# Kernel optimization log

Measured on AMD Instinct MI355X. Metric: run time of the kernel, lower is better.

The kernel has to match this reference:

```python
import jax, jax.numpy as jnp
import numpy as np
import math

INPUT_DIM = 256
HIDDEN_DIM = 128  # per-head dim
NUM_HEAD = 8
N = 1024          # seq len == variables
BATCH = 8
C = HIDDEN_DIM * NUM_HEAD  # 1024


def setup_inputs() -> dict:
    key = jax.random.key(0)
    ks = jax.random.split(key, 11)
    s = 0.02
    return {
        "x": jax.random.normal(ks[0], (BATCH, N, INPUT_DIM), dtype=jnp.float32),
        "B_bias": jax.random.normal(ks[1], (N, N), dtype=jnp.float32),
        "wq_w": jax.random.normal(ks[2], (INPUT_DIM, C), dtype=jnp.float32) * s,
        "wq_b": jax.random.normal(ks[3], (C,), dtype=jnp.float32) * s,
        "wk_w": jax.random.normal(ks[4], (INPUT_DIM, C), dtype=jnp.float32) * s,
        "wk_b": jax.random.normal(ks[5], (C,), dtype=jnp.float32) * s,
        "wv_w": jax.random.normal(ks[6], (INPUT_DIM, C), dtype=jnp.float32) * s,
        "wv_b": jax.random.normal(ks[7], (C,), dtype=jnp.float32) * s,
        "proj_w": jax.random.normal(ks[8], (C, HIDDEN_DIM), dtype=jnp.float32) * s,
        "proj_b": jax.random.normal(ks[9], (HIDDEN_DIM,), dtype=jnp.float32) * s,
    }


def reference(x, B_bias, wq_w, wq_b, wk_w, wk_b, wv_w, wv_b, proj_w, proj_b):
    B, n, _ = x.shape
    sdk = jnp.float32(math.sqrt(HIDDEN_DIM))
    # projections -> [B, N, C], split heads -> [B, H, N, h]
    def heads(y):
        return y.reshape(B, n, NUM_HEAD, HIDDEN_DIM).transpose(0, 2, 1, 3)
    q = heads(x @ wq_w + wq_b)
    k = heads(x @ wk_w + wk_b)
    v = heads(x @ wv_w + wv_b)
    # scores [B, H, N, N] with learned additive bias (broadcast over B, H)
    scores = jnp.einsum("bhnd,bhmd->bhnm", q, k) / sdk + B_bias
    attn = jax.nn.softmax(scores, axis=-1)
    out = jnp.einsum("bhnm,bhmd->bhnd", attn, v)  # [B, H, N, h]
    out = out.transpose(0, 2, 1, 3).reshape(B, n, C)
    return out @ proj_w + proj_b
```

## Files before the change

### kernel.cpp

```cpp
#include <hip/hip_runtime.h>
#include <math.h>

#define SEQ  1024
#define IND  256
#define CC   1024
#define NH   8
#define HD   128
#define BH   64

typedef __bf16 bf16x8 __attribute__((ext_vector_type(8)));
typedef __bf16 bf16x4 __attribute__((ext_vector_type(4)));
typedef float  f32x4  __attribute__((ext_vector_type(4)));
typedef unsigned short u16;

static constexpr float RSDK = 0.08838834764831845f;

__device__ __forceinline__ u16 f2bf(float f) {
    unsigned int u = __float_as_uint(f);
    u += 0x7fffu + ((u >> 16) & 1u);
    return (u16)(u >> 16);
}

__device__ __forceinline__ unsigned cvt_pk_bf16(float lo, float hi) {
    unsigned r;
    asm("v_cvt_pk_bf16_f32 %0, %1, %2" : "=v"(r) : "v"(lo), "v"(hi));
    return r;
}

__global__ __launch_bounds__(256) void prep_kernel(
    const float* __restrict__ x, u16* __restrict__ xb,
    const float* __restrict__ w0, const float* __restrict__ w1, const float* __restrict__ w2,
    u16* __restrict__ o0, u16* __restrict__ o1, u16* __restrict__ o2,
    const float* __restrict__ pw, u16* __restrict__ pT)
{
    __shared__ float tile[32][33];
    const int id = blockIdx.x;

    if (id < 2048) {
        const int i = id * 256 + threadIdx.x;
        float4 v = ((const float4*)x)[i];
        ushort4 o;
        o.x = f2bf(v.x); o.y = f2bf(v.y); o.z = f2bf(v.z); o.w = f2bf(v.w);
        ((ushort4*)xb)[i] = o;
        return;
    }

    const float* in; u16* out; int R, C, c0, r0;
    if (id < 2816) {
        const int rem = id - 2048;
        const int z = rem >> 8;
        const int rem2 = rem & 255;
        in  = (z == 0) ? w0 : (z == 1) ? w1 : w2;
        out = (z == 0) ? o0 : (z == 1) ? o1 : o2;
        R = IND; C = CC;
        c0 = (rem2 & 31) * 32;
        r0 = (rem2 >> 5) * 32;
    } else {
        const int rem = id - 2816;
        in = pw; out = pT;
        R = CC; C = HD;
        c0 = (rem & 3) * 32;
        r0 = (rem >> 2) * 32;
    }

    const int row = threadIdx.x >> 3, col4 = (threadIdx.x & 7) * 4;
    float4 v = *(const float4*)&in[(size_t)(r0 + row) * C + c0 + col4];
    tile[row][col4 + 0] = v.x; tile[row][col4 + 1] = v.y;
    tile[row][col4 + 2] = v.z; tile[row][col4 + 3] = v.w;
    __syncthreads();
    ushort4 o;
    o.x = f2bf(tile[col4 + 0][row]);
    o.y = f2bf(tile[col4 + 1][row]);
    o.z = f2bf(tile[col4 + 2][row]);
    o.w = f2bf(tile[col4 + 3][row]);
    *(ushort4*)&out[(size_t)(c0 + row) * R + r0 + col4] = o;
}

#define QKV_LDW 72
__global__ __launch_bounds__(256) void qkv_kernel(
    const u16* __restrict__ xb,
    const u16* __restrict__ wT0, const u16* __restrict__ wT1, const u16* __restrict__ wT2,
    const float* __restrict__ b0, const float* __restrict__ b1, const float* __restrict__ b2,
    u16* __restrict__ q_out, u16* __restrict__ k_out, u16* __restrict__ vt_out)
{
    const int mat = blockIdx.z;
    const u16* wT  = (mat == 0) ? wT0 : (mat == 1) ? wT1 : wT2;
    const float* wb = (mat == 0) ? b0 : (mat == 1) ? b1 : b2;
    const float scale = (mat == 0) ? RSDK : 1.0f;

    __shared__ __align__(16) u16 As[128 * QKV_LDW];
    __shared__ __align__(16) u16 Bs[128 * QKV_LDW];

    const int tid = threadIdx.x;
    const int lane = tid & 63, wave = tid >> 6;
    const int ln = lane & 15, quad = lane >> 4;
    const int m0 = blockIdx.x * 128;
    const int n0 = blockIdx.y * 128;
    const int wm = (wave & 1) * 64;
    const int wn = (wave >> 1) * 64;

    f32x4 acc[4][4];
    #pragma unroll
    for (int mb = 0; mb < 4; ++mb)
        #pragma unroll
        for (int nb = 0; nb < 4; ++nb)
            #pragma unroll
            for (int r = 0; r < 4; ++r) acc[mb][nb][r] = 0.0f;

    const int r8 = tid >> 3, pb8 = tid & 7;

    const u16* ag = xb + (size_t)(m0 + r8) * IND + pb8 * 8;
    const u16* bg = wT + (size_t)(n0 + r8) * IND + pb8 * 8;

    bf16x8 pa[4], pbv[4];
    #pragma unroll
    for (int c = 0; c < 4; ++c) {
        pa[c]  = *(const bf16x8*)(ag + (size_t)c * 32 * IND);
        pbv[c] = *(const bf16x8*)(bg + (size_t)c * 32 * IND);
    }

    for (int kt = 0; kt < 4; ++kt) {
        __syncthreads();
        #pragma unroll
        for (int c = 0; c < 4; ++c) {
            *(bf16x8*)(As + (size_t)(c * 32 + r8) * QKV_LDW + pb8 * 8) = pa[c];
            *(bf16x8*)(Bs + (size_t)(c * 32 + r8) * QKV_LDW + pb8 * 8) = pbv[c];
        }
        __syncthreads();
        if (kt < 3) {
            #pragma unroll
            for (int c = 0; c < 4; ++c) {
                pa[c]  = *(const bf16x8*)(ag + (size_t)c * 32 * IND + (kt + 1) * 64);
                pbv[c] = *(const bf16x8*)(bg + (size_t)c * 32 * IND + (kt + 1) * 64);
            }
        }
        #pragma unroll
        for (int ks = 0; ks < 2; ++ks) {
            bf16x8 af[4], bf[4];
            #pragma unroll
            for (int mb = 0; mb < 4; ++mb)
                af[mb] = *(const bf16x8*)(As + (size_t)(wm + mb * 16 + ln) * QKV_LDW
                                             + (ks * 4 + quad) * 8);
            #pragma unroll
            for (int nb = 0; nb < 4; ++nb)
                bf[nb] = *(const bf16x8*)(Bs + (size_t)(wn + nb * 16 + ln) * QKV_LDW
                                             + (ks * 4 + quad) * 8);
            #pragma unroll
            for (int mb = 0; mb < 4; ++mb)
                #pragma unroll
                for (int nb = 0; nb < 4; ++nb)
                    acc[mb][nb] = __builtin_amdgcn_mfma_f32_16x16x32_bf16(
                        af[mb], bf[nb], acc[mb][nb], 0, 0, 0);
        }
    }

    if (mat != 2) {
        u16* outp = (mat == 0) ? q_out : k_out;
        #pragma unroll
        for (int nb = 0; nb < 4; ++nb) {
            const int c = n0 + wn + nb * 16 + ln;
            const float bv = wb[c];
            const int h = c >> 7, d = c & 127;
            #pragma unroll
            for (int mb = 0; mb < 4; ++mb) {
                #pragma unroll
                for (int r = 0; r < 4; ++r) {
                    const int m = m0 + wm + mb * 16 + quad * 4 + r;
                    const int b = m >> 10, tok = m & 1023;
                    outp[((size_t)(b * NH + h) * SEQ + tok) * HD + d] =
                        f2bf((acc[mb][nb][r] + bv) * scale);
                }
            }
        }
    } else {
        #pragma unroll
        for (int nb = 0; nb < 4; ++nb) {
            const int c = n0 + wn + nb * 16 + ln;
            const float bv = wb[c];
            const int h = c >> 7, d = c & 127;
            #pragma unroll
            for (int mb = 0; mb < 4; ++mb) {
                const int m = m0 + wm + mb * 16 + quad * 4;
                const int b = m >> 10, tok0 = m & 1023;
                ushort4 o;
                o.x = f2bf(acc[mb][nb][0] + bv);
                o.y = f2bf(acc[mb][nb][1] + bv);
                o.z = f2bf(acc[mb][nb][2] + bv);
                o.w = f2bf(acc[mb][nb][3] + bv);
                *(ushort4*)&vt_out[((size_t)(b * NH + h) * HD + d) * SEQ + tok0] = o;
            }
        }
    }
}

#define KVB    32
#define KS_LDW 136
#define VS_LDW 40
__global__ __launch_bounds__(256, 2) void attn_kernel(
    const u16* __restrict__ Q, const u16* __restrict__ K,
    const u16* __restrict__ Vt, const float* __restrict__ bias,
    u16* __restrict__ aout)
{
    __shared__ __align__(16) u16 Ks[KVB * KS_LDW];
    __shared__ __align__(16) u16 Vs[128 * VS_LDW];

    const int tid = threadIdx.x;
    const int lane = tid & 63, wave = tid >> 6;
    const int ln = lane & 15, quad = lane >> 4;
    const int bh = blockIdx.x;
    const int q0 = blockIdx.y * 128 + wave * 32;

    bf16x8 qf[2][4];
    #pragma unroll
    for (int mb = 0; mb < 2; ++mb) {
        const u16* qp = Q + ((size_t)bh * SEQ + q0 + mb * 16 + ln) * HD + quad * 8;
        #pragma unroll
        for (int ks = 0; ks < 4; ++ks) qf[mb][ks] = *(const bf16x8*)(qp + ks * 32);
    }

    f32x4 Oa[2][8];
    #pragma unroll
    for (int mb = 0; mb < 2; ++mb)
        #pragma unroll
        for (int db = 0; db < 8; ++db)
            #pragma unroll
            for (int r = 0; r < 4; ++r) Oa[mb][db][r] = 0.0f;
    float l_loc[2] = {0.0f, 0.0f};

    const u16* Kg0 = K  + (size_t)bh * SEQ * HD;
    const u16* Vg0 = Vt + (size_t)bh * HD * SEQ;
    const float* brow0 = bias + (size_t)(q0 + ln) * SEQ + quad * 4;
    const float* brow1 = brow0 + (size_t)16 * SEQ;

    const int r16 = tid >> 4, pb16 = tid & 15;
    const int r4  = tid >> 2, pb4  = tid & 3;

    const u16* kg = Kg0 + (size_t)r16 * HD + pb16 * 8;
    const u16* vg = Vg0 + (size_t)r4 * SEQ + pb4 * 8;

    bf16x8 kp[2], vp[2];
    #pragma unroll
    for (int c = 0; c < 2; ++c) {
        kp[c] = *(const bf16x8*)(kg + (size_t)c * 16 * HD);
        vp[c] = *(const bf16x8*)(vg + (size_t)c * 64 * SEQ);
    }

    float4 bpre[2][2];
    #pragma unroll
    for (int mb = 0; mb < 2; ++mb)
        #pragma unroll
        for (int nb = 0; nb < 2; ++nb)
            bpre[mb][nb] = *(const float4*)((mb ? brow1 : brow0) + nb * 16);

    for (int kt = 0; kt < 32; ++kt) {
        __syncthreads();
        #pragma unroll
        for (int c = 0; c < 2; ++c) {
            *(bf16x8*)(Ks + (size_t)(c * 16 + r16) * KS_LDW + pb16 * 8) = kp[c];
            *(bf16x8*)(Vs + (size_t)(c * 64 + r4) * VS_LDW + pb4 * 8)   = vp[c];
        }
        __syncthreads();

        if (kt < 31) {
            #pragma unroll
            for (int c = 0; c < 2; ++c) {
                kp[c] = *(const bf16x8*)(kg + (size_t)(kt + 1) * KVB * HD + (size_t)c * 16 * HD);
                vp[c] = *(const bf16x8*)(vg + (size_t)c * 64 * SEQ + (kt + 1) * KVB);
            }
        }

        float p8[2][2][4];
        #pragma unroll
        for (int nb = 0; nb < 2; ++nb) {
            const u16* kr = Ks + (size_t)(nb * 16 + ln) * KS_LDW;
            bf16x8 kf[4];
            #pragma unroll
            for (int ks = 0; ks < 4; ++ks)
                kf[ks] = *(const bf16x8*)(kr + (ks * 4 + quad) * 8);
            #pragma unroll
            for (int mb = 0; mb < 2; ++mb) {
                f32x4 s;
                #pragma unroll
                for (int r = 0; r < 4; ++r) s[r] = 0.0f;
                #pragma unroll
                for (int ks = 0; ks < 4; ++ks)
                    s = __builtin_amdgcn_mfma_f32_16x16x32_bf16(kf[ks], qf[mb][ks], s, 0, 0, 0);
                #pragma unroll
                for (int r = 0; r < 4; ++r) {
                    const float p = __expf(s[r] + bpre[mb][nb][r]);
                    l_loc[mb] += p;
                    p8[mb][nb][r] = p;
                }
            }
        }

        if (kt < 31) {
            #pragma unroll
            for (int mb = 0; mb < 2; ++mb)
                #pragma unroll
                for (int nb = 0; nb < 2; ++nb)
                    bpre[mb][nb] = *(const float4*)((mb ? brow1 : brow0)
                                                    + (kt + 1) * KVB + nb * 16);
        }

        bf16x8 af[2];
        #pragma unroll
        for (int mb = 0; mb < 2; ++mb) {
            unsigned x0 = cvt_pk_bf16(p8[mb][0][0], p8[mb][0][1]);
            unsigned x1 = cvt_pk_bf16(p8[mb][0][2], p8[mb][0][3]);
            unsigned y0 = cvt_pk_bf16(p8[mb][1][0], p8[mb][1][1]);
            unsigned y1 = cvt_pk_bf16(p8[mb][1][2], p8[mb][1][3]);
            asm("v_permlane32_swap_b32 %0, %1" : "+v"(x0), "+v"(y0));
            asm("v_permlane32_swap_b32 %0, %1" : "+v"(x1), "+v"(y1));
            asm("v_permlane16_swap_b32 %0, %1" : "+v"(x0), "+v"(y0));
            asm("v_permlane16_swap_b32 %0, %1" : "+v"(x1), "+v"(y1));
            union { unsigned u[4]; bf16x8 v; } afu;
            afu.u[0] = x0; afu.u[1] = x1; afu.u[2] = y0; afu.u[3] = y1;
            af[mb] = afu.v;
        }

        #pragma unroll
        for (int db = 0; db < 8; ++db) {
            bf16x8 vf = *(const bf16x8*)(Vs + (size_t)(db * 16 + ln) * VS_LDW + quad * 8);
            #pragma unroll
            for (int mb = 0; mb < 2; ++mb)
                Oa[mb][db] = __builtin_amdgcn_mfma_f32_16x16x32_bf16(
                    af[mb], vf, Oa[mb][db], 0, 0, 0);
        }
    }

    const int b = bh >> 3, h = bh & 7;
    #pragma unroll
    for (int mb = 0; mb < 2; ++mb) {
        float ltot = l_loc[mb];
        ltot += __shfl_xor(ltot, 16);
        ltot += __shfl_xor(ltot, 32);
        #pragma unroll
        for (int r = 0; r < 4; ++r) {
            const float inv = 1.0f / __shfl(ltot, quad * 4 + r);
            const int tok = q0 + mb * 16 + quad * 4 + r;
            u16* op = aout + ((size_t)(b * SEQ + tok)) * CC + h * HD + ln;
            #pragma unroll
            for (int db = 0; db < 8; ++db) op[db * 16] = f2bf(Oa[mb][db][r] * inv);
        }
    }
}

__global__ __launch_bounds__(256) void proj_kernel(
    const u16* __restrict__ A, const u16* __restrict__ pT,
    const float* __restrict__ pb, float* __restrict__ out)
{
    __shared__ float Rs[3][16 * 132];
    const int tid = threadIdx.x;
    const int lane = tid & 63, kh = tid >> 6;
    const int ln = lane & 15, quad = lane >> 4;
    const int m0 = blockIdx.x * 16;

    f32x4 acc[8];
    #pragma unroll
    for (int nb = 0; nb < 8; ++nb)
        #pragma unroll
        for (int r = 0; r < 4; ++r) acc[nb][r] = 0.0f;

    const u16* ap = A  + (size_t)(m0 + ln) * CC + kh * 256 + quad * 8;
    const u16* bp = pT + (size_t)ln * CC + kh * 256 + quad * 8;

    #pragma unroll
    for (int kt = 0; kt < 8; ++kt) {
        bf16x8 af = *(const bf16x8*)(ap + kt * 32);
        #pragma unroll
        for (int nb = 0; nb < 8; ++nb) {
            bf16x8 bf = *(const bf16x8*)(bp + (size_t)nb * 16 * CC + kt * 32);
            acc[nb] = __builtin_amdgcn_mfma_f32_16x16x32_bf16(af, bf, acc[nb], 0, 0, 0);
        }
    }

    if (kh > 0) {
        #pragma unroll
        for (int nb = 0; nb < 8; ++nb)
            #pragma unroll
            for (int r = 0; r < 4; ++r)
                Rs[kh - 1][(quad * 4 + r) * 132 + nb * 16 + ln] = acc[nb][r];
    }
    __syncthreads();
    if (kh == 0) {
        #pragma unroll
        for (int nb = 0; nb < 8; ++nb) {
            const int c = nb * 16 + ln;
            const float bv = pb[c];
            #pragma unroll
            for (int r = 0; r < 4; ++r) {
                const int ri = (quad * 4 + r) * 132 + c;
                out[(size_t)(m0 + quad * 4 + r) * HD + c] =
                    acc[nb][r] + Rs[0][ri] + Rs[1][ri] + Rs[2][ri] + bv;
            }
        }
    }
}

extern "C" void kernel_launch(void* const* d_in, const int* in_sizes, int n_in,
                              void* d_out, int out_size, void* d_ws, size_t ws_size,
                              hipStream_t stream)
{
    const float* x    = (const float*)d_in[0];
    const float* bias = (const float*)d_in[1];
    const float* wq   = (const float*)d_in[2];
    const float* wqb  = (const float*)d_in[3];
    const float* wk   = (const float*)d_in[4];
    const float* wkb  = (const float*)d_in[5];
    const float* wv   = (const float*)d_in[6];
    const float* wvb  = (const float*)d_in[7];
    const float* pw   = (const float*)d_in[8];
    const float* pb   = (const float*)d_in[9];
    float* out = (float*)d_out;

    u16* ws = (u16*)d_ws;
    size_t off = 0;
    u16* xb  = ws + off; off += (size_t)8192 * IND;
    u16* wqT = ws + off; off += (size_t)CC * IND;
    u16* wkT = ws + off; off += (size_t)CC * IND;
    u16* wvT = ws + off; off += (size_t)CC * IND;
    u16* pT  = ws + off; off += (size_t)HD * CC;
    u16* Qw  = ws + off; off += (size_t)BH * SEQ * HD;
    u16* Kw  = ws + off; off += (size_t)BH * SEQ * HD;
    u16* Vtw = ws + off; off += (size_t)BH * HD * SEQ;
    u16* Aw  = ws + off; off += (size_t)8192 * CC;

    prep_kernel<<<2944, 256, 0, stream>>>(x, xb, wq, wk, wv, wqT, wkT, wvT, pw, pT);
    qkv_kernel<<<dim3(64, 8, 3), 256, 0, stream>>>(
        xb, wqT, wkT, wvT, wqb, wkb, wvb, Qw, Kw, Vtw);
    attn_kernel<<<dim3(64, 8), 256, 0, stream>>>(Qw, Kw, Vtw, bias, Aw);
    proj_kernel<<<512, 256, 0, stream>>>(Aw, pT, pb, out);
}
```

Baseline: 172.1 us.

## Split attention KV loop across two wave groups and merge partial outputs in LDS

The attention block doubles to 512 threads, with two groups of four waves each handling alternating KV tiles over the same query rows. This halves the serial KV loop per wave and adds more waves for latency hiding. At the end, group 1 writes its partial O and row sums to shared memory and group 0 adds them before the store. The change relies on the softmax having no max subtraction, so partials add directly. It costs a reduction through LDS and tighter register limits under launch_bounds(512,4).

```diff
diff --git a/kernel.cpp b/kernel.cpp
--- a/kernel.cpp
+++ b/kernel.cpp
@@ -196,19 +196,25 @@
 #define KVB    32
 #define KS_LDW 136
 #define VS_LDW 40
-__global__ __launch_bounds__(256, 2) void attn_kernel(
+#define KS_SZ  (KVB * KS_LDW)
+#define VS_SZ  (128 * VS_LDW)
+__global__ __launch_bounds__(512, 4) void attn_kernel(
     const u16* __restrict__ Q, const u16* __restrict__ K,
     const u16* __restrict__ Vt, const float* __restrict__ bias,
     u16* __restrict__ aout)
 {
-    __shared__ __align__(16) u16 Ks[KVB * KS_LDW];
-    __shared__ __align__(16) u16 Vs[128 * VS_LDW];
+    __shared__ __align__(16) u16 SM[2 * KS_SZ + 2 * VS_SZ];
 
     const int tid = threadIdx.x;
     const int lane = tid & 63, wave = tid >> 6;
     const int ln = lane & 15, quad = lane >> 4;
+    const int g  = wave >> 2;
+    const int wq = wave & 3;
     const int bh = blockIdx.x;
-    const int q0 = blockIdx.y * 128 + wave * 32;
+    const int q0 = blockIdx.y * 128 + wq * 32;
+
+    u16* Ksg = SM + g * KS_SZ;
+    u16* Vsg = SM + 2 * KS_SZ + g * VS_SZ;
 
     bf16x8 qf[2][4];
     #pragma unroll
@@ -232,47 +238,46 @@
     const float* brow0 = bias + (size_t)(q0 + ln) * SEQ + quad * 4;
     const float* brow1 = brow0 + (size_t)16 * SEQ;
 
-    const int r16 = tid >> 4, pb16 = tid & 15;
-    const int r4  = tid >> 2, pb4  = tid & 3;
+    const int st = tid & 255;
+    const int r16 = st >> 4, pb16 = st & 15;
+    const int r4  = st >> 2, pb4  = st & 3;
 
     const u16* kg = Kg0 + (size_t)r16 * HD + pb16 * 8;
     const u16* vg = Vg0 + (size_t)r4 * SEQ + pb4 * 8;
 
     bf16x8 kp[2], vp[2];
-    #pragma unroll
-    for (int c = 0; c < 2; ++c) {
-        kp[c] = *(const bf16x8*)(kg + (size_t)c * 16 * HD);
-        vp[c] = *(const bf16x8*)(vg + (size_t)c * 64 * SEQ);
-    }
+    kp[0] = *(const bf16x8*)(kg + (size_t)g * KVB * HD);
+    kp[1] = *(const bf16x8*)(kg + (size_t)g * KVB * HD + (size_t)16 * HD);
+    vp[0] = *(const bf16x8*)(vg + g * KVB);
+    vp[1] = *(const bf16x8*)(vg + (size_t)64 * SEQ + g * KVB);
 
     float4 bpre[2][2];
     #pragma unroll
     for (int mb = 0; mb < 2; ++mb)
         #pragma unroll
         for (int nb = 0; nb < 2; ++nb)
-            bpre[mb][nb] = *(const float4*)((mb ? brow1 : brow0) + nb * 16);
-
-    for (int kt = 0; kt < 32; ++kt) {
-        __syncthreads();
-        #pragma unroll
-        for (int c = 0; c < 2; ++c) {
-            *(bf16x8*)(Ks + (size_t)(c * 16 + r16) * KS_LDW + pb16 * 8) = kp[c];
-            *(bf16x8*)(Vs + (size_t)(c * 64 + r4) * VS_LDW + pb4 * 8)   = vp[c];
-        }
-        __syncthreads();
-
-        if (kt < 31) {
-            #pragma unroll
-            for (int c = 0; c < 2; ++c) {
-                kp[c] = *(const bf16x8*)(kg + (size_t)(kt + 1) * KVB * HD + (size_t)c * 16 * HD);
-                vp[c] = *(const bf16x8*)(vg + (size_t)c * 64 * SEQ + (kt + 1) * KVB);
-            }
+            bpre[mb][nb] = *(const float4*)((mb ? brow1 : brow0) + g * KVB + nb * 16);
+
+    for (int i = 0; i < 16; ++i) {
+        __syncthreads();
+        *(bf16x8*)(Ksg + (size_t)r16 * KS_LDW + pb16 * 8)        = kp[0];
+        *(bf16x8*)(Ksg + (size_t)(16 + r16) * KS_LDW + pb16 * 8) = kp[1];
+        *(bf16x8*)(Vsg + (size_t)r4 * VS_LDW + pb4 * 8)          = vp[0];
+        *(bf16x8*)(Vsg + (size_t)(64 + r4) * VS_LDW + pb4 * 8)   = vp[1];
+        __syncthreads();
+
+        if (i < 15) {
+            const size_t t = (size_t)(2 * (i + 1) + g);
+            kp[0] = *(const bf16x8*)(kg + t * KVB * HD);
+            kp[1] = *(const bf16x8*)(kg + t * KVB * HD + (size_t)16 * HD);
+            vp[0] = *(const bf16x8*)(vg + t * KVB);
+            vp[1] = *(const bf16x8*)(vg + (size_t)64 * SEQ + t * KVB);
         }
 
         float p8[2][2][4];
         #pragma unroll
         for (int nb = 0; nb < 2; ++nb) {
-            const u16* kr = Ks + (size_t)(nb * 16 + ln) * KS_LDW;
+            const u16* kr = Ksg + (size_t)(nb * 16 + ln) * KS_LDW;
             bf16x8 kf[4];
             #pragma unroll
             for (int ks = 0; ks < 4; ++ks)
@@ -294,13 +299,14 @@
             }
         }
 
-        if (kt < 31) {
+        if (i < 15) {
+            const int t = 2 * (i + 1) + g;
             #pragma unroll
             for (int mb = 0; mb < 2; ++mb)
                 #pragma unroll
                 for (int nb = 0; nb < 2; ++nb)
                     bpre[mb][nb] = *(const float4*)((mb ? brow1 : brow0)
-                                                    + (kt + 1) * KVB + nb * 16);
+                                                    + t * KVB + nb * 16);
         }
 
         bf16x8 af[2];
@@ -321,13 +327,37 @@
 
         #pragma unroll
         for (int db = 0; db < 8; ++db) {
-            bf16x8 vf = *(const bf16x8*)(Vs + (size_t)(db * 16 + ln) * VS_LDW + quad * 8);
+            bf16x8 vf = *(const bf16x8*)(Vsg + (size_t)(db * 16 + ln) * VS_LDW + quad * 8);
             #pragma unroll
             for (int mb = 0; mb < 2; ++mb)
                 Oa[mb][db] = __builtin_amdgcn_mfma_f32_16x16x32_bf16(
                     af[mb], vf, Oa[mb][db], 0, 0, 0);
         }
     }
+
+    float* M = (float*)SM;
+    #pragma unroll
+    for (int mb = 0; mb < 2; ++mb) {
+        __syncthreads();
+        float* mp = M + (size_t)(wq * 64 + lane) * 34;
+        if (g == 1) {
+            #pragma unroll
+            for (int db = 0; db < 8; ++db)
+                #pragma unroll
+                for (int r = 0; r < 4; ++r) mp[db * 4 + r] = Oa[mb][db][r];
+            mp[32] = l_loc[mb];
+        }
+        __syncthreads();
+        if (g == 0) {
+            #pragma unroll
+            for (int db = 0; db < 8; ++db)
+                #pragma unroll
+                for (int r = 0; r < 4; ++r) Oa[mb][db][r] += mp[db * 4 + r];
+            l_loc[mb] += mp[32];
+        }
+    }
+
+    if (g != 0) return;
 
     const int b = bh >> 3, h = bh & 7;
     #pragma unroll
@@ -429,6 +459,6 @@
     prep_kernel<<<2944, 256, 0, stream>>>(x, xb, wq, wk, wv, wqT, wkT, wvT, pw, pT);
     qkv_kernel<<<dim3(64, 8, 3), 256, 0, stream>>>(
         xb, wqT, wkT, wvT, wqb, wkb, wvb, Qw, Kw, Vtw);
-    attn_kernel<<<dim3(64, 8), 256, 0, stream>>>(Qw, Kw, Vtw, bias, Aw);
+    attn_kernel<<<dim3(64, 8), 512, 0, stream>>>(Qw, Kw, Vtw, bias, Aw);
     proj_kernel<<<512, 256, 0, stream>>>(Aw, pT, pb, out);
 }
```

Result: slower. 245.8 us (+42.9%).

## Load QKV GEMM tiles directly to LDS and vectorize Q/K stores via operand swap

Applied to the files above, without the earlier changes.

The QKV projection GEMM now stages A/B tiles with global_load_lds (direct global-to-LDS) in place of register prefetch plus ds_write, and drops the padded LDS stride. For the Q and K outputs, the MFMA operands are swapped so each lane holds four consecutive head-dim values, which allows packed 8-byte stores and float4 bias loads instead of scalar 2-byte scattered stores. The trade-off is losing the register double-buffering overlap (loads are now synchronous per k-step) and possible LDS bank conflicts from the unpadded 64-element row stride.

```diff
diff --git a/kernel.cpp b/kernel.cpp
--- a/kernel.cpp
+++ b/kernel.cpp
@@ -25,6 +25,12 @@
     unsigned r;
     asm("v_cvt_pk_bf16_f32 %0, %1, %2" : "=v"(r) : "v"(lo), "v"(hi));
     return r;
+}
+
+__device__ __forceinline__ void gload16(const u16* g, u16* l) {
+    __builtin_amdgcn_global_load_lds(
+        (const __attribute__((address_space(1))) unsigned int*)g,
+        (__attribute__((address_space(3))) unsigned int*)l, 16, 0, 0);
 }
 
 __global__ __launch_bounds__(256) void prep_kernel(
@@ -76,7 +82,6 @@
     *(ushort4*)&out[(size_t)(c0 + row) * R + r0 + col4] = o;
 }
 
-#define QKV_LDW 72
 __global__ __launch_bounds__(256) void qkv_kernel(
     const u16* __restrict__ xb,
     const u16* __restrict__ wT0, const u16* __restrict__ wT1, const u16* __restrict__ wT2,
@@ -88,8 +93,8 @@
     const float* wb = (mat == 0) ? b0 : (mat == 1) ? b1 : b2;
     const float scale = (mat == 0) ? RSDK : 1.0f;
 
-    __shared__ __align__(16) u16 As[128 * QKV_LDW];
-    __shared__ __align__(16) u16 Bs[128 * QKV_LDW];
+    __shared__ __align__(16) u16 As[128 * 64];
+    __shared__ __align__(16) u16 Bs[128 * 64];
 
     const int tid = threadIdx.x;
     const int lane = tid & 63, wave = tid >> 6;
@@ -107,69 +112,71 @@
             #pragma unroll
             for (int r = 0; r < 4; ++r) acc[mb][nb][r] = 0.0f;
 
-    const int r8 = tid >> 3, pb8 = tid & 7;
-
-    const u16* ag = xb + (size_t)(m0 + r8) * IND + pb8 * 8;
-    const u16* bg = wT + (size_t)(n0 + r8) * IND + pb8 * 8;
-
-    bf16x8 pa[4], pbv[4];
-    #pragma unroll
-    for (int c = 0; c < 4; ++c) {
-        pa[c]  = *(const bf16x8*)(ag + (size_t)c * 32 * IND);
-        pbv[c] = *(const bf16x8*)(bg + (size_t)c * 32 * IND);
-    }
+    const int grow = lane >> 3;
+    const int gcol = (lane & 7) * 8;
 
     for (int kt = 0; kt < 4; ++kt) {
         __syncthreads();
         #pragma unroll
         for (int c = 0; c < 4; ++c) {
-            *(bf16x8*)(As + (size_t)(c * 32 + r8) * QKV_LDW + pb8 * 8) = pa[c];
-            *(bf16x8*)(Bs + (size_t)(c * 32 + r8) * QKV_LDW + pb8 * 8) = pbv[c];
+            const int rb = (wave * 4 + c) * 8;
+            gload16(xb + (size_t)(m0 + rb + grow) * IND + kt * 64 + gcol,
+                    As + (size_t)(wave * 4 + c) * 512);
+            gload16(wT + (size_t)(n0 + rb + grow) * IND + kt * 64 + gcol,
+                    Bs + (size_t)(wave * 4 + c) * 512);
         }
         __syncthreads();
-        if (kt < 3) {
-            #pragma unroll
-            for (int c = 0; c < 4; ++c) {
-                pa[c]  = *(const bf16x8*)(ag + (size_t)c * 32 * IND + (kt + 1) * 64);
-                pbv[c] = *(const bf16x8*)(bg + (size_t)c * 32 * IND + (kt + 1) * 64);
-            }
-        }
+
         #pragma unroll
         for (int ks = 0; ks < 2; ++ks) {
             bf16x8 af[4], bf[4];
             #pragma unroll
             for (int mb = 0; mb < 4; ++mb)
-                af[mb] = *(const bf16x8*)(As + (size_t)(wm + mb * 16 + ln) * QKV_LDW
+                af[mb] = *(const bf16x8*)(As + (size_t)(wm + mb * 16 + ln) * 64
                                              + (ks * 4 + quad) * 8);
             #pragma unroll
             for (int nb = 0; nb < 4; ++nb)
-                bf[nb] = *(const bf16x8*)(Bs + (size_t)(wn + nb * 16 + ln) * QKV_LDW
+                bf[nb] = *(const bf16x8*)(Bs + (size_t)(wn + nb * 16 + ln) * 64
                                              + (ks * 4 + quad) * 8);
-            #pragma unroll
-            for (int mb = 0; mb < 4; ++mb)
-                #pragma unroll
-                for (int nb = 0; nb < 4; ++nb)
-                    acc[mb][nb] = __builtin_amdgcn_mfma_f32_16x16x32_bf16(
-                        af[mb], bf[nb], acc[mb][nb], 0, 0, 0);
+            if (mat != 2) {
+                #pragma unroll
+                for (int mb = 0; mb < 4; ++mb)
+                    #pragma unroll
+                    for (int nb = 0; nb < 4; ++nb)
+                        acc[mb][nb] = __builtin_amdgcn_mfma_f32_16x16x32_bf16(
+                            bf[nb], af[mb], acc[mb][nb], 0, 0, 0);
+            } else {
+                #pragma unroll
+                for (int mb = 0; mb < 4; ++mb)
+                    #pragma unroll
+                    for (int nb = 0; nb < 4; ++nb)
+                        acc[mb][nb] = __builtin_amdgcn_mfma_f32_16x16x32_bf16(
+                            af[mb], bf[nb], acc[mb][nb], 0, 0, 0);
+            }
         }
     }
 
     if (mat != 2) {
         u16* outp = (mat == 0) ? q_out : k_out;
-        #pragma unroll
-        for (int nb = 0; nb < 4; ++nb) {
-            const int c = n0 + wn + nb * 16 + ln;
-            const float bv = wb[c];
-            const int h = c >> 7, d = c & 127;
-            #pragma unroll
-            for (int mb = 0; mb < 4; ++mb) {
-                #pragma unroll
-                for (int r = 0; r < 4; ++r) {
-                    const int m = m0 + wm + mb * 16 + quad * 4 + r;
-                    const int b = m >> 10, tok = m & 1023;
-                    outp[((size_t)(b * NH + h) * SEQ + tok) * HD + d] =
-                        f2bf((acc[mb][nb][r] + bv) * scale);
-                }
+        const int h = n0 >> 7;
+        float4 bv[4];
+        #pragma unroll
+        for (int nb = 0; nb < 4; ++nb)
+            bv[nb] = *(const float4*)&wb[n0 + wn + nb * 16 + quad * 4];
+        #pragma unroll
+        for (int mb = 0; mb < 4; ++mb) {
+            const int m = m0 + wm + mb * 16 + ln;
+            const int b = m >> 10, tok = m & 1023;
+            u16* orow = outp + ((size_t)(b * NH + h) * SEQ + tok) * HD;
+            #pragma unroll
+            for (int nb = 0; nb < 4; ++nb) {
+                const int d0 = wn + nb * 16 + quad * 4;
+                ushort4 o;
+                o.x = f2bf((acc[mb][nb][0] + bv[nb].x) * scale);
+                o.y = f2bf((acc[mb][nb][1] + bv[nb].y) * scale);
+                o.z = f2bf((acc[mb][nb][2] + bv[nb].z) * scale);
+                o.w = f2bf((acc[mb][nb][3] + bv[nb].w) * scale);
+                *(ushort4*)&orow[d0] = o;
             }
         }
     } else {
```

Result: slower. 179.7 us (+4.4%).

## Double attention KV tile to 64 and vectorize Q/K projection stores

Applied to the files above, without the earlier changes.

The attention kernel now processes 64 keys per iteration instead of 32, which halves the number of loop iterations and barrier pairs and doubles the work between synchronizations. The cost is more registers for K/V prefetch, bias and probabilities, plus larger LDS tiles. The QKV projection kernel swaps the MFMA operand order for Q and K so each lane holds four consecutive head-dim elements, turning scalar 2-byte scattered stores into 8-byte vector stores with a vectorized bias load.

```diff
diff --git a/kernel.cpp b/kernel.cpp
--- a/kernel.cpp
+++ b/kernel.cpp
@@ -145,31 +145,45 @@
             for (int nb = 0; nb < 4; ++nb)
                 bf[nb] = *(const bf16x8*)(Bs + (size_t)(wn + nb * 16 + ln) * QKV_LDW
                                              + (ks * 4 + quad) * 8);
-            #pragma unroll
-            for (int mb = 0; mb < 4; ++mb)
-                #pragma unroll
-                for (int nb = 0; nb < 4; ++nb)
-                    acc[mb][nb] = __builtin_amdgcn_mfma_f32_16x16x32_bf16(
-                        af[mb], bf[nb], acc[mb][nb], 0, 0, 0);
+            if (mat != 2) {
+                #pragma unroll
+                for (int mb = 0; mb < 4; ++mb)
+                    #pragma unroll
+                    for (int nb = 0; nb < 4; ++nb)
+                        acc[mb][nb] = __builtin_amdgcn_mfma_f32_16x16x32_bf16(
+                            bf[nb], af[mb], acc[mb][nb], 0, 0, 0);
+            } else {
+                #pragma unroll
+                for (int mb = 0; mb < 4; ++mb)
+                    #pragma unroll
+                    for (int nb = 0; nb < 4; ++nb)
+                        acc[mb][nb] = __builtin_amdgcn_mfma_f32_16x16x32_bf16(
+                            af[mb], bf[nb], acc[mb][nb], 0, 0, 0);
+            }
         }
     }
 
     if (mat != 2) {
         u16* outp = (mat == 0) ? q_out : k_out;
-        #pragma unroll
-        for (int nb = 0; nb < 4; ++nb) {
-            const int c = n0 + wn + nb * 16 + ln;
-            const float bv = wb[c];
-            const int h = c >> 7, d = c & 127;
-            #pragma unroll
-            for (int mb = 0; mb < 4; ++mb) {
-                #pragma unroll
-                for (int r = 0; r < 4; ++r) {
-                    const int m = m0 + wm + mb * 16 + quad * 4 + r;
-                    const int b = m >> 10, tok = m & 1023;
-                    outp[((size_t)(b * NH + h) * SEQ + tok) * HD + d] =
-                        f2bf((acc[mb][nb][r] + bv) * scale);
-                }
+        const int h = n0 >> 7;
+        float4 bv[4];
+        #pragma unroll
+        for (int nb = 0; nb < 4; ++nb)
+            bv[nb] = *(const float4*)&wb[n0 + wn + nb * 16 + quad * 4];
+        #pragma unroll
+        for (int mb = 0; mb < 4; ++mb) {
+            const int m = m0 + wm + mb * 16 + ln;
+            const int b = m >> 10, tok = m & 1023;
+            u16* orow = outp + ((size_t)(b * NH + h) * SEQ + tok) * HD;
+            #pragma unroll
+            for (int nb = 0; nb < 4; ++nb) {
+                const int d0 = wn + nb * 16 + quad * 4;
+                ushort4 o;
+                o.x = f2bf((acc[mb][nb][0] + bv[nb].x) * scale);
+                o.y = f2bf((acc[mb][nb][1] + bv[nb].y) * scale);
+                o.z = f2bf((acc[mb][nb][2] + bv[nb].z) * scale);
+                o.w = f2bf((acc[mb][nb][3] + bv[nb].w) * scale);
+                *(ushort4*)&orow[d0] = o;
             }
         }
     } else {
@@ -193,9 +207,9 @@
     }
 }
 
-#define KVB    32
+#define KVB    64
 #define KS_LDW 136
-#define VS_LDW 40
+#define VS_LDW 72
 __global__ __launch_bounds__(256, 2) void attn_kernel(
     const u16* __restrict__ Q, const u16* __restrict__ K,
     const u16* __restrict__ Vt, const float* __restrict__ bias,
@@ -233,45 +247,45 @@
     const float* brow1 = brow0 + (size_t)16 * SEQ;
 
     const int r16 = tid >> 4, pb16 = tid & 15;
-    const int r4  = tid >> 2, pb4  = tid & 3;
+    const int r8  = tid >> 3, pb8  = tid & 7;
 
     const u16* kg = Kg0 + (size_t)r16 * HD + pb16 * 8;
-    const u16* vg = Vg0 + (size_t)r4 * SEQ + pb4 * 8;
-
-    bf16x8 kp[2], vp[2];
-    #pragma unroll
-    for (int c = 0; c < 2; ++c) {
+    const u16* vg = Vg0 + (size_t)r8 * SEQ + pb8 * 8;
+
+    bf16x8 kp[4], vp[4];
+    #pragma unroll
+    for (int c = 0; c < 4; ++c) {
         kp[c] = *(const bf16x8*)(kg + (size_t)c * 16 * HD);
-        vp[c] = *(const bf16x8*)(vg + (size_t)c * 64 * SEQ);
-    }
-
-    float4 bpre[2][2];
+        vp[c] = *(const bf16x8*)(vg + (size_t)c * 32 * SEQ);
+    }
+
+    float4 bpre[2][4];
     #pragma unroll
     for (int mb = 0; mb < 2; ++mb)
         #pragma unroll
-        for (int nb = 0; nb < 2; ++nb)
+        for (int nb = 0; nb < 4; ++nb)
             bpre[mb][nb] = *(const float4*)((mb ? brow1 : brow0) + nb * 16);
 
-    for (int kt = 0; kt < 32; ++kt) {
+    for (int kt = 0; kt < 16; ++kt) {
         __syncthreads();
         #pragma unroll
-        for (int c = 0; c < 2; ++c) {
+        for (int c = 0; c < 4; ++c) {
             *(bf16x8*)(Ks + (size_t)(c * 16 + r16) * KS_LDW + pb16 * 8) = kp[c];
-            *(bf16x8*)(Vs + (size_t)(c * 64 + r4) * VS_LDW + pb4 * 8)   = vp[c];
+            *(bf16x8*)(Vs + (size_t)(c * 32 + r8) * VS_LDW + pb8 * 8)   = vp[c];
         }
         __syncthreads();
 
-        if (kt < 31) {
-            #pragma unroll
-            for (int c = 0; c < 2; ++c) {
+        if (kt < 15) {
+            #pragma unroll
+            for (int c = 0; c < 4; ++c) {
                 kp[c] = *(const bf16x8*)(kg + (size_t)(kt + 1) * KVB * HD + (size_t)c * 16 * HD);
-                vp[c] = *(const bf16x8*)(vg + (size_t)c * 64 * SEQ + (kt + 1) * KVB);
-            }
-        }
-
-        float p8[2][2][4];
-        #pragma unroll
-        for (int nb = 0; nb < 2; ++nb) {
+                vp[c] = *(const bf16x8*)(vg + (size_t)c * 32 * SEQ + (kt + 1) * KVB);
+            }
+        }
+
+        float p8[2][4][4];
+        #pragma unroll
+        for (int nb = 0; nb < 4; ++nb) {
             const u16* kr = Ks + (size_t)(nb * 16 + ln) * KS_LDW;
             bf16x8 kf[4];
             #pragma unroll
@@ -294,38 +308,44 @@
             }
         }
 
-        if (kt < 31) {
+        if (kt < 15) {
             #pragma unroll
             for (int mb = 0; mb < 2; ++mb)
                 #pragma unroll
-                for (int nb = 0; nb < 2; ++nb)
+                for (int nb = 0; nb < 4; ++nb)
                     bpre[mb][nb] = *(const float4*)((mb ? brow1 : brow0)
                                                     + (kt + 1) * KVB + nb * 16);
         }
 
-        bf16x8 af[2];
-        #pragma unroll
-        for (int mb = 0; mb < 2; ++mb) {
-            unsigned x0 = cvt_pk_bf16(p8[mb][0][0], p8[mb][0][1]);
-            unsigned x1 = cvt_pk_bf16(p8[mb][0][2], p8[mb][0][3]);
-            unsigned y0 = cvt_pk_bf16(p8[mb][1][0], p8[mb][1][1]);
-            unsigned y1 = cvt_pk_bf16(p8[mb][1][2], p8[mb][1][3]);
-            asm("v_permlane32_swap_b32 %0, %1" : "+v"(x0), "+v"(y0));
-            asm("v_permlane32_swap_b32 %0, %1" : "+v"(x1), "+v"(y1));
-            asm("v_permlane16_swap_b32 %0, %1" : "+v"(x0), "+v"(y0));
-            asm("v_permlane16_swap_b32 %0, %1" : "+v"(x1), "+v"(y1));
-            union { unsigned u[4]; bf16x8 v; } afu;
-            afu.u[0] = x0; afu.u[1] = x1; afu.u[2] = y0; afu.u[3] = y1;
-            af[mb] = afu.v;
-        }
+        bf16x8 af[2][2];
+        #pragma unroll
+        for (int mb = 0; mb < 2; ++mb)
+            #pragma unroll
+            for (int h2 = 0; h2 < 2; ++h2) {
+                unsigned x0 = cvt_pk_bf16(p8[mb][2 * h2][0], p8[mb][2 * h2][1]);
+                unsigned x1 = cvt_pk_bf16(p8[mb][2 * h2][2], p8[mb][2 * h2][3]);
+                unsigned y0 = cvt_pk_bf16(p8[mb][2 * h2 + 1][0], p8[mb][2 * h2 + 1][1]);
+                unsigned y1 = cvt_pk_bf16(p8[mb][2 * h2 + 1][2], p8[mb][2 * h2 + 1][3]);
+                asm("v_permlane32_swap_b32 %0, %1" : "+v"(x0), "+v"(y0));
+                asm("v_permlane32_swap_b32 %0, %1" : "+v"(x1), "+v"(y1));
+                asm("v_permlane16_swap_b32 %0, %1" : "+v"(x0), "+v"(y0));
+                asm("v_permlane16_swap_b32 %0, %1" : "+v"(x1), "+v"(y1));
+                union { unsigned u[4]; bf16x8 v; } afu;
+                afu.u[0] = x0; afu.u[1] = x1; afu.u[2] = y0; afu.u[3] = y1;
+                af[mb][h2] = afu.v;
+            }
 
         #pragma unroll
         for (int db = 0; db < 8; ++db) {
-            bf16x8 vf = *(const bf16x8*)(Vs + (size_t)(db * 16 + ln) * VS_LDW + quad * 8);
-            #pragma unroll
-            for (int mb = 0; mb < 2; ++mb)
-                Oa[mb][db] = __builtin_amdgcn_mfma_f32_16x16x32_bf16(
-                    af[mb], vf, Oa[mb][db], 0, 0, 0);
+            #pragma unroll
+            for (int h2 = 0; h2 < 2; ++h2) {
+                bf16x8 vf = *(const bf16x8*)(Vs + (size_t)(db * 16 + ln) * VS_LDW
+                                                + h2 * 32 + quad * 8);
+                #pragma unroll
+                for (int mb = 0; mb < 2; ++mb)
+                    Oa[mb][db] = __builtin_amdgcn_mfma_f32_16x16x32_bf16(
+                        af[mb][h2], vf, Oa[mb][db], 0, 0, 0);
+            }
         }
     }
 
```

Result: slower. 179.3 us (+4.2%).
